# Kernel optimization log

Measured on AMD Instinct MI355X. Metric: run time of the kernel, lower is better.

## Reference

```python
import jax, jax.numpy as jnp
import numpy as np
import math

B, S, H = 4, 2048, 1024
EMBED_DIM = 1024


def setup_inputs() -> dict:
    key = jax.random.key(0)
    ks = jax.random.split(key, 7)
    scale = 1.0 / math.sqrt(H)
    return {
        "xs": jax.random.normal(ks[0], (B, S, H), dtype=jnp.float32),
        "WQ_w": jax.random.normal(ks[1], (EMBED_DIM, H), dtype=jnp.float32) * scale,
        "WQ_b": jax.random.normal(ks[2], (EMBED_DIM,), dtype=jnp.float32) * scale,
        "WK_w": jax.random.normal(ks[3], (EMBED_DIM, H), dtype=jnp.float32) * scale,
        "WK_b": jax.random.normal(ks[4], (EMBED_DIM,), dtype=jnp.float32) * scale,
        "WV_w": jax.random.normal(ks[5], (EMBED_DIM, H), dtype=jnp.float32) * scale,
        "WV_b": jax.random.normal(ks[6], (EMBED_DIM,), dtype=jnp.float32) * scale,
    }


def reference(xs, WQ_w, WQ_b, WK_w, WK_b, WV_w, WV_b):
    # Linear projections (torch nn.Linear: x @ W.T + b)
    q = jnp.einsum('bsh,eh->bse', xs, WQ_w) + WQ_b  # [B,S,E]
    k = jnp.einsum('bsh,eh->bse', xs, WK_w) + WK_b
    v = jnp.einsum('bsh,eh->bse', xs, WV_w) + WV_b
    seq_len = xs.shape[1]
    inv_sqrt_e = 1.0 / math.sqrt(EMBED_DIM)
    qk = jnp.einsum('bqe,bke->bqk', q, k) * inv_sqrt_e  # [B,S,S]
    # causal mask: positions k > q get -inf (triu, diagonal=1)
    causal = jnp.tril(jnp.ones((seq_len, seq_len), dtype=bool))
    qk = jnp.where(causal[None, :, :], qk, -jnp.inf)
    attn = jax.nn.softmax(qk, axis=2)
    y = jnp.einsum('bqk,bke->bqe', attn, v)  # [B,S,E]
    return y
```

## Files before the change

### kernel.cpp

```cpp
#include <hip/hip_runtime.h>
#include <cstdint>
#include <cstddef>

typedef _Float16 f16;
typedef __attribute__((ext_vector_type(4))) _Float16 f16x4;
typedef __attribute__((ext_vector_type(8))) _Float16 f16x8;
typedef __attribute__((ext_vector_type(4))) float f32x4;

static constexpr int BB = 4;
static constexpr int SS = 2048;
static constexpr int EE = 1024;

static constexpr int BM = 128, BN = 128;

__device__ __forceinline__ void gload_lds16(const f16* g, f16* l) {
  __builtin_amdgcn_global_load_lds(
      (const __attribute__((address_space(1))) void*)g,
      (__attribute__((address_space(3))) void*)l, 16, 0, 0);
}

struct Frag {
  int lane, wave, wy, wx, l16, quad, quadx;
  __device__ Frag() {
    const int tid = threadIdx.x;
    lane = tid & 63; wave = tid >> 6;
    wy = wave >> 1; wx = wave & 1;
    l16 = lane & 15; quad = lane >> 4;
    quadx = quad ^ ((l16 >> 2) & 3);
  }
};

struct Stager {
  const f16* g[2];
  int l[2];
  __device__ void init(const f16* base, int ld, const Frag& fr) {
#pragma unroll
    for (int i = 0; i < 2; ++i) {
      const int c = fr.wave * 128 + i * 64 + fr.lane;
      const int row = c >> 2;
      const int kcs = (c & 3) ^ ((c >> 4) & 3);
      g[i] = base + (size_t)row * ld + kcs * 8;
      l[i] = c * 8;
    }
  }
  __device__ __forceinline__ void stage(int ko, f16* lds) const {
    gload_lds16(g[0] + ko, lds + l[0]);
    gload_lds16(g[1] + ko, lds + l[1]);
  }
};

__device__ __forceinline__ void mfma_round(
    const f16* __restrict__ Ash, const f16* __restrict__ Bsh,
    f32x4 acc[4][4], const Frag& fr)
{
  f16x8 af[4], bf[4];
#pragma unroll
  for (int mi = 0; mi < 4; ++mi)
    af[mi] = *(const f16x8*)(Ash + (fr.wy * 64 + mi * 16 + fr.l16) * 32 + fr.quadx * 8);
#pragma unroll
  for (int ni = 0; ni < 4; ++ni)
    bf[ni] = *(const f16x8*)(Bsh + (fr.wx * 64 + ni * 16 + fr.l16) * 32 + fr.quadx * 8);
#pragma unroll
  for (int mi = 0; mi < 4; ++mi)
#pragma unroll
    for (int ni = 0; ni < 4; ++ni)
      acc[mi][ni] = __builtin_amdgcn_mfma_f32_16x16x32_f16(af[mi], bf[ni], acc[mi][ni], 0, 0, 0);
}

__device__ __forceinline__ void gemm_core(
    const f16* __restrict__ A, const f16* __restrict__ Bt,
    int lda, int ldb, int kOuter,
    f16* __restrict__ Ash, f16* __restrict__ Bsh,
    f32x4 acc[4][4], const Frag& fr)
{
  Stager sa, sb;
  sa.init(A, lda, fr);
  sb.init(Bt, ldb, fr);
  for (int kt = 0; kt < kOuter; ++kt) {
    const int ko = kt * 64;
    sa.stage(ko, Ash);       sa.stage(ko + 32, Ash + 128 * 32);
    sb.stage(ko, Bsh);       sb.stage(ko + 32, Bsh + 128 * 32);
    __syncthreads();
    mfma_round(Ash, Bsh, acc, fr);
    mfma_round(Ash + 128 * 32, Bsh + 128 * 32, acc, fr);
    __syncthreads();
  }
}

__global__ __launch_bounds__(256) void cast_kernel(
    const float* __restrict__ in, f16* __restrict__ out, int n4)
{
  const int i = blockIdx.x * 256 + threadIdx.x;
  if (i < n4) {
    const float4 f = ((const float4*)in)[i];
    f16x4 h;
    h.x = (f16)f.x; h.y = (f16)f.y; h.z = (f16)f.z; h.w = (f16)f.w;
    ((f16x4*)out)[i] = h;
  }
}

__global__ __launch_bounds__(256) void cast_w_kernel(
    const float* __restrict__ w0, const float* __restrict__ w1, const float* __restrict__ w2,
    f16* __restrict__ o0, f16* __restrict__ o1, f16* __restrict__ o2, int n4)
{
  const int z = blockIdx.y;
  const float* in = (z == 0) ? w0 : (z == 1) ? w1 : w2;
  f16* out = (z == 0) ? o0 : (z == 1) ? o1 : o2;
  const int i = blockIdx.x * 256 + threadIdx.x;
  if (i < n4) {
    const float4 f = ((const float4*)in)[i];
    f16x4 h;
    h.x = (f16)f.x; h.y = (f16)f.y; h.z = (f16)f.z; h.w = (f16)f.w;
    ((f16x4*)out)[i] = h;
  }
}

__global__ __launch_bounds__(256, 2) void qkv_fused_kernel(
    const f16* __restrict__ X,
    const f16* __restrict__ W0, const f16* __restrict__ W1, const f16* __restrict__ W2,
    const float* __restrict__ b0, const float* __restrict__ b1, const float* __restrict__ b2,
    f16* __restrict__ O0, f16* __restrict__ O1, f16* __restrict__ O2)
{
  __shared__ __align__(16) f16 Ash[2][BM * 32];
  __shared__ __align__(16) f16 Bsh[3][2][BN * 32];
  const int row0 = blockIdx.x * BM, col0 = blockIdx.y * BN;
  Frag fr;

  Stager sa, sw[3];
  sa.init(X + (size_t)row0 * EE, EE, fr);
  sw[0].init(W0 + (size_t)col0 * EE, EE, fr);
  sw[1].init(W1 + (size_t)col0 * EE, EE, fr);
  sw[2].init(W2 + (size_t)col0 * EE, EE, fr);

  f32x4 acc[3][4][4] = {};

  for (int kt = 0; kt < EE / 64; ++kt) {
    const int ko = kt * 64;
    sa.stage(ko, Ash[0]);  sa.stage(ko + 32, Ash[1]);
#pragma unroll
    for (int z = 0; z < 3; ++z) {
      sw[z].stage(ko, Bsh[z][0]);  sw[z].stage(ko + 32, Bsh[z][1]);
    }
    __syncthreads();
#pragma unroll
    for (int h = 0; h < 2; ++h) {
      f16x8 af[4];
#pragma unroll
      for (int mi = 0; mi < 4; ++mi)
        af[mi] = *(const f16x8*)(Ash[h] + (fr.wy * 64 + mi * 16 + fr.l16) * 32 + fr.quadx * 8);
#pragma unroll
      for (int z = 0; z < 3; ++z) {
        f16x8 bf[4];
#pragma unroll
        for (int ni = 0; ni < 4; ++ni)
          bf[ni] = *(const f16x8*)(Bsh[z][h] + (fr.wx * 64 + ni * 16 + fr.l16) * 32 + fr.quadx * 8);
#pragma unroll
        for (int mi = 0; mi < 4; ++mi)
#pragma unroll
          for (int ni = 0; ni < 4; ++ni)
            acc[z][mi][ni] = __builtin_amdgcn_mfma_f32_16x16x32_f16(af[mi], bf[ni], acc[z][mi][ni], 0, 0, 0);
      }
    }
    __syncthreads();
  }

#pragma unroll
  for (int z = 0; z < 3; ++z) {
    const float* bias = (z == 0) ? b0 : (z == 1) ? b1 : b2;
    f16* out = (z == 0) ? O0 : (z == 1) ? O1 : O2;
#pragma unroll
    for (int ni = 0; ni < 4; ++ni) {
      const int c = col0 + fr.wx * 64 + ni * 16 + fr.l16;
      const float bv = bias[c];
#pragma unroll
      for (int mi = 0; mi < 4; ++mi) {
        const int r = row0 + fr.wy * 64 + mi * 16 + fr.quad * 4;
#pragma unroll
        for (int i = 0; i < 4; ++i)
          out[(size_t)(r + i) * EE + c] = (f16)(acc[z][mi][ni][i] + bv);
      }
    }
  }
}

__global__ __launch_bounds__(256) void transpose_kernel(
    const f16* __restrict__ V, f16* __restrict__ Vt)
{
  __shared__ __align__(16) f16 t[64][68];
  const int b = blockIdx.z;
  const int s0 = blockIdx.x * 64, e0 = blockIdx.y * 64;
  const int tid = threadIdx.x;
  const int r = tid >> 4;
  const int c4 = (tid & 15) << 2;
  const f16* src = V + (size_t)b * SS * EE;
  f16* dst = Vt + (size_t)b * EE * SS;
#pragma unroll
  for (int i = 0; i < 4; ++i) {
    const int row = i * 16 + r;
    const f16x4 v = *(const f16x4*)(src + (size_t)(s0 + row) * EE + e0 + c4);
    *(f16x4*)&t[row][c4] = v;
  }
  __syncthreads();
#pragma unroll
  for (int i = 0; i < 4; ++i) {
    const int row = i * 16 + r;
    f16x4 v;
    v.x = t[c4 + 0][row]; v.y = t[c4 + 1][row];
    v.z = t[c4 + 2][row]; v.w = t[c4 + 3][row];
    *(f16x4*)(dst + (size_t)(e0 + row) * SS + s0 + c4) = v;
  }
}

__global__ __launch_bounds__(256) void scores_kernel(
    const f16* __restrict__ Q, const f16* __restrict__ Kh, f16* __restrict__ Sc)
{
  __shared__ __align__(16) f16 Ash[2][BM * 32];
  __shared__ __align__(16) f16 Bsh[2][BN * 32];
  const int t = blockIdx.x, b = blockIdx.z;
  int qt = 0;
  while ((qt + 1) * (qt + 2) / 2 <= t) ++qt;
  const int kt = t - qt * (qt + 1) / 2;
  const f16* A  = Q  + (size_t)b * SS * EE + (size_t)qt * BM * EE;
  const f16* Bp = Kh + (size_t)b * SS * EE + (size_t)kt * BN * EE;
  f16* out = Sc + (size_t)b * SS * SS;
  Frag fr;
  f32x4 acc[4][4] = {};
  gemm_core(A, Bp, EE, EE, EE / 64, Ash[0], Bsh[0], acc, fr);
  const float scale = 0.03125f;
#pragma unroll
  for (int ni = 0; ni < 4; ++ni) {
    const int c = kt * BN + fr.wx * 64 + ni * 16 + fr.l16;
#pragma unroll
    for (int mi = 0; mi < 4; ++mi) {
      const int r = qt * BM + fr.wy * 64 + mi * 16 + fr.quad * 4;
#pragma unroll
      for (int i = 0; i < 4; ++i)
        out[(size_t)(r + i) * SS + c] = (f16)(acc[mi][ni][i] * scale);
    }
  }
}

__global__ __launch_bounds__(256) void softmax_kernel(f16* __restrict__ Sc)
{
  const int q = blockIdx.x, b = blockIdx.y;
  f16* row = Sc + (size_t)b * SS * SS + (size_t)q * SS;
  const int n = q + 1;
  const int kend = ((q >> 7) + 1) << 7;
  const int tid = threadIdx.x;
  const int i0 = tid * 8;

  float v[8];
  if (i0 + 8 <= n) {
    const f16x8 h = *(const f16x8*)(row + i0);
#pragma unroll
    for (int j = 0; j < 8; ++j) v[j] = (float)h[j];
  } else {
#pragma unroll
    for (int j = 0; j < 8; ++j) {
      const int idx = i0 + j;
      v[j] = (idx < n) ? (float)row[idx] : -1e30f;
    }
  }

  float m = v[0];
#pragma unroll
  for (int j = 1; j < 8; ++j) m = fmaxf(m, v[j]);
  __shared__ float red[4];
#pragma unroll
  for (int off = 32; off > 0; off >>= 1) m = fmaxf(m, __shfl_down(m, off));
  if ((tid & 63) == 0) red[tid >> 6] = m;
  __syncthreads();
  m = fmaxf(fmaxf(red[0], red[1]), fmaxf(red[2], red[3]));

  float sum = 0.f;
#pragma unroll
  for (int j = 0; j < 8; ++j) {
    v[j] = (i0 + j < n) ? __expf(v[j] - m) : 0.f;
    sum += v[j];
  }
#pragma unroll
  for (int off = 32; off > 0; off >>= 1) sum += __shfl_down(sum, off);
  __syncthreads();
  if ((tid & 63) == 0) red[tid >> 6] = sum;
  __syncthreads();
  sum = red[0] + red[1] + red[2] + red[3];
  const float inv = 1.f / sum;

  if (i0 < kend) {
    f16x8 h;
#pragma unroll
    for (int j = 0; j < 8; ++j) h[j] = (f16)(v[j] * inv);
    *(f16x8*)(row + i0) = h;
  }
}

__global__ __launch_bounds__(256) void pv_kernel(
    const f16* __restrict__ P, const f16* __restrict__ Vt, float* __restrict__ Y)
{
  __shared__ __align__(16) f16 Ash[2][BM * 32];
  __shared__ __align__(16) f16 Bsh[2][BN * 32];
  const int qt = (gridDim.x - 1) - blockIdx.x, et = blockIdx.y, b = blockIdx.z;
  const f16* A  = P  + (size_t)b * SS * SS + (size_t)qt * BM * SS;
  const f16* Bp = Vt + (size_t)b * EE * SS + (size_t)et * BN * SS;
  float* out = Y + (size_t)b * SS * EE;
  Frag fr;
  f32x4 acc[4][4] = {};
  gemm_core(A, Bp, SS, SS, (qt + 1) * 2, Ash[0], Bsh[0], acc, fr);
#pragma unroll
  for (int ni = 0; ni < 4; ++ni) {
    const int c = et * BN + fr.wx * 64 + ni * 16 + fr.l16;
#pragma unroll
    for (int mi = 0; mi < 4; ++mi) {
      const int r = qt * BM + fr.wy * 64 + mi * 16 + fr.quad * 4;
#pragma unroll
      for (int i = 0; i < 4; ++i)
        out[(size_t)(r + i) * EE + c] = acc[mi][ni][i];
    }
  }
}

extern "C" void kernel_launch(void* const* d_in, const int* in_sizes, int n_in,
                              void* d_out, int out_size, void* d_ws, size_t ws_size,
                              hipStream_t stream)
{
  const float* xs  = (const float*)d_in[0];
  const float* WQw = (const float*)d_in[1];
  const float* WQb = (const float*)d_in[2];
  const float* WKw = (const float*)d_in[3];
  const float* WKb = (const float*)d_in[4];
  const float* WVw = (const float*)d_in[5];
  const float* WVb = (const float*)d_in[6];

  const size_t ME = (size_t)BB * SS * EE;
  const size_t WE = (size_t)EE * EE;

  f16* Xh = (f16*)d_ws;
  f16* Wq = Xh + ME;
  f16* Wk = Wq + WE;
  f16* Wv = Wk + WE;
  f16* Qh = Wv + WE;
  f16* Kh = Qh + ME;
  f16* Vh = Kh + ME;
  f16* Vt = Vh + ME;
  f16* Sc = Vt + ME;

  cast_kernel<<<dim3((unsigned)(ME / 4 / 256)), 256, 0, stream>>>(xs, Xh, (int)(ME / 4));
  cast_w_kernel<<<dim3((unsigned)(WE / 4 / 256), 3), 256, 0, stream>>>(
      WQw, WKw, WVw, Wq, Wk, Wv, (int)(WE / 4));

  qkv_fused_kernel<<<dim3((BB * SS) / BM, EE / BN), 256, 0, stream>>>(
      Xh, Wq, Wk, Wv, WQb, WKb, WVb, Qh, Kh, Vh);
  transpose_kernel<<<dim3(SS / 64, EE / 64, BB), 256, 0, stream>>>(Vh, Vt);
  const int nTri = (SS / BM) * (SS / BM + 1) / 2;
  scores_kernel<<<dim3(nTri, 1, BB), 256, 0, stream>>>(Qh, Kh, Sc);
  softmax_kernel<<<dim3(SS, BB), 256, 0, stream>>>(Sc);
  pv_kernel<<<dim3(SS / BM, EE / BN, BB), 256, 0, stream>>>(Sc, Vt, (float*)d_out);
}
```

Baseline: 258.7 us.

## Compute V transposed directly via Wv·X^T GEMM, dropping transpose kernel

Splits the fused QKV projection into a Q/K fused GEMM and a separate GEMM that computes Vt = Wv·X^T with bias, writing V already transposed. This removes the separate transpose kernel and the intermediate V buffer round trip through memory. The tradeoff is that X is read twice (once per GEMM), and the Vt epilogue writes strided scalar f16 stores along the sequence dimension.

```diff
diff --git a/kernel.cpp b/kernel.cpp
--- a/kernel.cpp
+++ b/kernel.cpp
@@ -115,30 +115,29 @@
   }
 }
 
-__global__ __launch_bounds__(256, 2) void qkv_fused_kernel(
+__global__ __launch_bounds__(256, 2) void qk_fused_kernel(
     const f16* __restrict__ X,
-    const f16* __restrict__ W0, const f16* __restrict__ W1, const f16* __restrict__ W2,
-    const float* __restrict__ b0, const float* __restrict__ b1, const float* __restrict__ b2,
-    f16* __restrict__ O0, f16* __restrict__ O1, f16* __restrict__ O2)
+    const f16* __restrict__ W0, const f16* __restrict__ W1,
+    const float* __restrict__ b0, const float* __restrict__ b1,
+    f16* __restrict__ O0, f16* __restrict__ O1)
 {
   __shared__ __align__(16) f16 Ash[2][BM * 32];
-  __shared__ __align__(16) f16 Bsh[3][2][BN * 32];
+  __shared__ __align__(16) f16 Bsh[2][2][BN * 32];
   const int row0 = blockIdx.x * BM, col0 = blockIdx.y * BN;
   Frag fr;
 
-  Stager sa, sw[3];
+  Stager sa, sw[2];
   sa.init(X + (size_t)row0 * EE, EE, fr);
   sw[0].init(W0 + (size_t)col0 * EE, EE, fr);
   sw[1].init(W1 + (size_t)col0 * EE, EE, fr);
-  sw[2].init(W2 + (size_t)col0 * EE, EE, fr);
-
-  f32x4 acc[3][4][4] = {};
+
+  f32x4 acc[2][4][4] = {};
 
   for (int kt = 0; kt < EE / 64; ++kt) {
     const int ko = kt * 64;
     sa.stage(ko, Ash[0]);  sa.stage(ko + 32, Ash[1]);
 #pragma unroll
-    for (int z = 0; z < 3; ++z) {
+    for (int z = 0; z < 2; ++z) {
       sw[z].stage(ko, Bsh[z][0]);  sw[z].stage(ko + 32, Bsh[z][1]);
     }
     __syncthreads();
@@ -149,7 +148,7 @@
       for (int mi = 0; mi < 4; ++mi)
         af[mi] = *(const f16x8*)(Ash[h] + (fr.wy * 64 + mi * 16 + fr.l16) * 32 + fr.quadx * 8);
 #pragma unroll
-      for (int z = 0; z < 3; ++z) {
+      for (int z = 0; z < 2; ++z) {
         f16x8 bf[4];
 #pragma unroll
         for (int ni = 0; ni < 4; ++ni)
@@ -165,9 +164,9 @@
   }
 
 #pragma unroll
-  for (int z = 0; z < 3; ++z) {
-    const float* bias = (z == 0) ? b0 : (z == 1) ? b1 : b2;
-    f16* out = (z == 0) ? O0 : (z == 1) ? O1 : O2;
+  for (int z = 0; z < 2; ++z) {
+    const float* bias = (z == 0) ? b0 : b1;
+    f16* out = (z == 0) ? O0 : O1;
 #pragma unroll
     for (int ni = 0; ni < 4; ++ni) {
       const int c = col0 + fr.wx * 64 + ni * 16 + fr.l16;
@@ -183,31 +182,30 @@
   }
 }
 
-__global__ __launch_bounds__(256) void transpose_kernel(
-    const f16* __restrict__ V, f16* __restrict__ Vt)
-{
-  __shared__ __align__(16) f16 t[64][68];
-  const int b = blockIdx.z;
-  const int s0 = blockIdx.x * 64, e0 = blockIdx.y * 64;
-  const int tid = threadIdx.x;
-  const int r = tid >> 4;
-  const int c4 = (tid & 15) << 2;
-  const f16* src = V + (size_t)b * SS * EE;
-  f16* dst = Vt + (size_t)b * EE * SS;
-#pragma unroll
-  for (int i = 0; i < 4; ++i) {
-    const int row = i * 16 + r;
-    const f16x4 v = *(const f16x4*)(src + (size_t)(s0 + row) * EE + e0 + c4);
-    *(f16x4*)&t[row][c4] = v;
-  }
-  __syncthreads();
-#pragma unroll
-  for (int i = 0; i < 4; ++i) {
-    const int row = i * 16 + r;
-    f16x4 v;
-    v.x = t[c4 + 0][row]; v.y = t[c4 + 1][row];
-    v.z = t[c4 + 2][row]; v.w = t[c4 + 3][row];
-    *(f16x4*)(dst + (size_t)(e0 + row) * SS + s0 + c4) = v;
+__global__ __launch_bounds__(256, 2) void vt_gemm_kernel(
+    const f16* __restrict__ Wv, const f16* __restrict__ X,
+    const float* __restrict__ bv, f16* __restrict__ Vt)
+{
+  __shared__ __align__(16) f16 Ash[2][BM * 32];
+  __shared__ __align__(16) f16 Bsh[2][BN * 32];
+  const int row0 = blockIdx.x * BM;
+  const int sg0 = blockIdx.y * BN;
+  const int b = sg0 / SS, s0 = sg0 % SS;
+  Frag fr;
+  f32x4 acc[4][4] = {};
+  gemm_core(Wv + (size_t)row0 * EE, X + (size_t)sg0 * EE, EE, EE, EE / 64,
+            Ash[0], Bsh[0], acc, fr);
+  f16* out = Vt + (size_t)b * EE * SS;
+#pragma unroll
+  for (int ni = 0; ni < 4; ++ni) {
+    const int c = s0 + fr.wx * 64 + ni * 16 + fr.l16;
+#pragma unroll
+    for (int mi = 0; mi < 4; ++mi) {
+      const int r = row0 + fr.wy * 64 + mi * 16 + fr.quad * 4;
+#pragma unroll
+      for (int i = 0; i < 4; ++i)
+        out[(size_t)(r + i) * SS + c] = (f16)(acc[mi][ni][i] + bv[r + i]);
+    }
   }
 }
 
@@ -340,17 +338,17 @@
   f16* Wv = Wk + WE;
   f16* Qh = Wv + WE;
   f16* Kh = Qh + ME;
-  f16* Vh = Kh + ME;
-  f16* Vt = Vh + ME;
+  f16* Vt = Kh + ME;
   f16* Sc = Vt + ME;
 
   cast_kernel<<<dim3((unsigned)(ME / 4 / 256)), 256, 0, stream>>>(xs, Xh, (int)(ME / 4));
   cast_w_kernel<<<dim3((unsigned)(WE / 4 / 256), 3), 256, 0, stream>>>(
       WQw, WKw, WVw, Wq, Wk, Wv, (int)(WE / 4));
 
-  qkv_fused_kernel<<<dim3((BB * SS) / BM, EE / BN), 256, 0, stream>>>(
-      Xh, Wq, Wk, Wv, WQb, WKb, WVb, Qh, Kh, Vh);
-  transpose_kernel<<<dim3(SS / 64, EE / 64, BB), 256, 0, stream>>>(Vh, Vt);
+  qk_fused_kernel<<<dim3((BB * SS) / BM, EE / BN), 256, 0, stream>>>(
+      Xh, Wq, Wk, WQb, WKb, Qh, Kh);
+  vt_gemm_kernel<<<dim3(EE / BM, (BB * SS) / BN), 256, 0, stream>>>(
+      Wv, Xh, WVb, Vt);
   const int nTri = (SS / BM) * (SS / BM + 1) / 2;
   scores_kernel<<<dim3(nTri, 1, BB), 256, 0, stream>>>(Qh, Kh, Sc);
   softmax_kernel<<<dim3(SS, BB), 256, 0, stream>>>(Sc);
```

Result: no change. 262.4 us (+1.4%).
